# Optimization experiments

Hardware: AMD Instinct MI355X
Metric: run time of the kernel (lower is better)

The kernel has to match this reference:

```python
import jax, jax.numpy as jnp
import numpy as np

DIM = 2048
N_HEADS = 16
N_KV_HEADS = 4
HEAD_DIM = DIM // N_HEADS  # 128
B, S = 2, 2048


def setup_inputs() -> dict:
    key = jax.random.key(0)
    ks = jax.random.split(key, 7)
    x = jax.random.normal(ks[0], (B, S, DIM), dtype=jnp.float32)
    # rotary tables: freqs_cis = exp(i * t * theta), theta_j = 1/10000^(2j/head_dim)
    inv_freq = 1.0 / (10000.0 ** (np.arange(0, HEAD_DIM, 2, dtype=np.float32) / HEAD_DIM))
    t = np.arange(S, dtype=np.float32)
    angles = jnp.asarray(np.outer(t, inv_freq))  # [S, HEAD_DIM//2]
    freqs_cos = jnp.cos(angles)
    freqs_sin = jnp.sin(angles)
    # Linear weights stored [in, out] (torch Linear applies x @ W.T; equivalent math)
    sd = 1.0 / np.sqrt(DIM)
    wq = jax.random.uniform(ks[1], (DIM, N_HEADS * HEAD_DIM), jnp.float32, -sd, sd)
    wk = jax.random.uniform(ks[2], (DIM, N_KV_HEADS * HEAD_DIM), jnp.float32, -sd, sd)
    wv = jax.random.uniform(ks[3], (DIM, N_KV_HEADS * HEAD_DIM), jnp.float32, -sd, sd)
    wo = jax.random.uniform(ks[4], (N_HEADS * HEAD_DIM, DIM), jnp.float32, -sd, sd)
    return {"x": x, "freqs_cos": freqs_cos, "freqs_sin": freqs_sin,
            "wq": wq, "wk": wk, "wv": wv, "wo": wo}


def _apply_rotary(xq, xk, cos, sin):
    # xq: [B,S,H,D], xk: [B,S,KH,D]; cos/sin: [S, D//2]
    def rot(t):
        tr = t.reshape(*t.shape[:-1], -1, 2)  # [..., D//2, 2] (real, imag)
        r, i = tr[..., 0], tr[..., 1]
        c = cos[None, :, None, :]
        s = sin[None, :, None, :]
        out_r = r * c - i * s
        out_i = r * s + i * c
        return jnp.stack([out_r, out_i], axis=-1).reshape(t.shape)
    return rot(xq), rot(xk)


def reference(x, freqs_cos, freqs_sin, wq, wk, wv, wo):
    bsz, seqlen, _ = x.shape
    xq = (x @ wq).reshape(bsz, seqlen, N_HEADS, HEAD_DIM)
    xk = (x @ wk).reshape(bsz, seqlen, N_KV_HEADS, HEAD_DIM)
    xv = (x @ wv).reshape(bsz, seqlen, N_KV_HEADS, HEAD_DIM)
    xq, xk = _apply_rotary(xq, xk, freqs_cos, freqs_sin)
    rep = N_HEADS // N_KV_HEADS
    xk = jnp.repeat(xk, rep, axis=2)
    xv = jnp.repeat(xv, rep, axis=2)
    # [B,H,S,D]
    q = xq.transpose(0, 2, 1, 3)
    k = xk.transpose(0, 2, 1, 3)
    v = xv.transpose(0, 2, 1, 3)
    scale = 1.0 / jnp.sqrt(jnp.asarray(HEAD_DIM, dtype=q.dtype))
    scores = jnp.einsum('bhqd,bhkd->bhqk', q, k) * scale
    causal = jnp.tril(jnp.ones((seqlen, seqlen), dtype=bool))
    scores = jnp.where(causal[None, None], scores, jnp.asarray(-jnp.inf, scores.dtype))
    attn = jax.nn.softmax(scores, axis=-1)
    out = jnp.einsum('bhqk,bhkd->bhqd', attn, v)  # [B,H,S,D]
    out = out.transpose(0, 2, 1, 3).reshape(bsz, seqlen, N_HEADS * HEAD_DIM)
    return out @ wo
```

## Files before the change

### kernel.cpp

```cpp
#include <hip/hip_runtime.h>
#include <hip/hip_bf16.h>

typedef unsigned short u16;
typedef unsigned int u32;
typedef __bf16 bf16x8 __attribute__((ext_vector_type(8)));
typedef float f32x4 __attribute__((ext_vector_type(4)));
typedef u32 u32x2 __attribute__((ext_vector_type(2)));

#define AS1 __attribute__((address_space(1)))
#define AS3 __attribute__((address_space(3)))

__device__ __forceinline__ void gload16(const void* gp, void* lp) {
    __builtin_amdgcn_global_load_lds((const AS1 u32*)gp, (AS3 u32*)lp, 16, 0, 0);
}

__device__ __forceinline__ u16 f2b(float f) {
    __bf16 h = (__bf16)f;
    return __builtin_bit_cast(u16, h);
}

__global__ __launch_bounds__(256) void prep_kernel(const float* __restrict__ x,
                                                   const float* __restrict__ wq,
                                                   const float* __restrict__ wk,
                                                   const float* __restrict__ wv,
                                                   const float* __restrict__ wo,
                                                   u16* __restrict__ xb,
                                                   u16* __restrict__ wT,
                                                   u16* __restrict__ woT) {
    __shared__ u16 tile[32][33];
    const int bid = blockIdx.x, tid = threadIdx.x;
    if (bid < 8192) {
        int i = bid * 256 + tid;
        f32x4 v = *(const f32x4*)(x + (size_t)i * 4);
        u32x2 o;
        o[0] = (u32)f2b(v[0]) | ((u32)f2b(v[1]) << 16);
        o[1] = (u32)f2b(v[2]) | ((u32)f2b(v[3]) << 16);
        *(u32x2*)(xb + (size_t)i * 4) = o;
        return;
    }
    const float* in;
    u16* out;
    int C, t;
    if (bid < 12288) { t = bid - 8192; in = wq; out = wT; C = 2048; }
    else if (bid < 13312) { t = bid - 12288; in = wk; out = wT + 2048 * 2048; C = 512; }
    else if (bid < 14336) { t = bid - 13312; in = wv; out = wT + 2560 * 2048; C = 512; }
    else { t = bid - 14336; in = wo; out = woT; C = 2048; }
    const int nbx = C >> 5;
    const int bx = (t % nbx) * 32, by = (t / nbx) * 32;
    const int tx = tid & 31, ty = tid >> 5;
#pragma unroll
    for (int i = 0; i < 32; i += 8)
        tile[ty + i][tx] = f2b(in[(size_t)(by + ty + i) * C + bx + tx]);
    __syncthreads();
#pragma unroll
    for (int i = 0; i < 32; i += 8)
        out[(size_t)(bx + ty + i) * 2048 + by + tx] = tile[tx][ty + i];
}

__global__ __launch_bounds__(256) void transpose_v(const u16* __restrict__ qkv,
                                                   u16* __restrict__ vT) {
    __shared__ u16 tile[32][33];
    const int bx = blockIdx.x * 32;
    const int by = blockIdx.y * 32;
    const int tx = threadIdx.x & 31, ty = threadIdx.x >> 5;
#pragma unroll
    for (int i = 0; i < 32; i += 8)
        tile[ty + i][tx] = qkv[(size_t)(by + ty + i) * 3072 + 2560 + bx + tx];
    __syncthreads();
    const int b = by >> 11, s0 = by & 2047;
#pragma unroll
    for (int i = 0; i < 32; i += 8)
        vT[(size_t)(b * 512 + bx + ty + i) * 2048 + s0 + tx] = tile[tx][ty + i];
}

template <typename OT, bool ROPE>
__global__ __launch_bounds__(256) void gemm_bt(const __bf16* __restrict__ A,
                                               const __bf16* __restrict__ Bt,
                                               OT* __restrict__ C,
                                               int K, int ldc,
                                               const float* __restrict__ fc,
                                               const float* __restrict__ fs) {
    __shared__ __align__(16) __bf16 Al[128 * 32];
    __shared__ __align__(16) __bf16 Bl[128 * 32];
    const int tid = threadIdx.x;
    const int lane = tid & 63, w = tid >> 6;
    const int wm = w >> 1, wn = w & 1;
    const int ln15 = lane & 15, lg = lane >> 4;
    const int nwg = gridDim.x * gridDim.y;
    const int lid = blockIdx.y * gridDim.x + blockIdx.x;
    const int swz = (lid & 7) * (nwg >> 3) + (lid >> 3);
    const int bm = swz / gridDim.x, bn = swz % gridDim.x;

    const f32x4 fzero = {0.f, 0.f, 0.f, 0.f};
    f32x4 acc[4][4];
#pragma unroll
    for (int m = 0; m < 4; m++)
#pragma unroll
        for (int n = 0; n < 4; n++) acc[m][n] = fzero;

    const __bf16* Ab = A + (size_t)(bm * 128) * K;
    const __bf16* Bb = Bt + (size_t)(bn * 128) * K;

    for (int k0 = 0; k0 < K; k0 += 32) {
#pragma unroll
        for (int i = 0; i < 2; i++) {
            int gid = i * 256 + tid;
            int row = gid >> 2, gc = gid & 3;
            gload16(Ab + (size_t)row * K + k0 + gc * 8, (char*)Al + gid * 16);
            gload16(Bb + (size_t)row * K + k0 + gc * 8, (char*)Bl + gid * 16);
        }
        __syncthreads();
        bf16x8 af[4], bfr[4];
#pragma unroll
        for (int m = 0; m < 4; m++)
            af[m] = *(const bf16x8*)&Al[(wm * 64 + m * 16 + ln15) * 32 + lg * 8];
#pragma unroll
        for (int n = 0; n < 4; n++)
            bfr[n] = *(const bf16x8*)&Bl[(wn * 64 + n * 16 + ln15) * 32 + lg * 8];
#pragma unroll
        for (int m = 0; m < 4; m++)
#pragma unroll
            for (int n = 0; n < 4; n++)
                acc[m][n] = __builtin_amdgcn_mfma_f32_16x16x32_bf16(af[m], bfr[n], acc[m][n], 0, 0, 0);
        __syncthreads();
    }

    if (ROPE) {
#pragma unroll
        for (int n = 0; n < 4; n++) {
            const int col = bn * 128 + wn * 64 + n * 16 + ln15;
            if (col < 2560) {
                const int p = (col & 127) >> 1;
                const bool odd = (col & 1) != 0;
#pragma unroll
                for (int m = 0; m < 4; m++)
#pragma unroll
                    for (int r = 0; r < 4; r++) {
                        const int row = bm * 128 + wm * 64 + m * 16 + lg * 4 + r;
                        const int sp = row & 2047;
                        float c = fc[sp * 64 + p];
                        float sn = fs[sp * 64 + p];
                        float v = acc[m][n][r];
                        float v2 = __shfl_xor(v, 1);
                        acc[m][n][r] = odd ? (v2 * sn + v * c) : (v * c - v2 * sn);
                    }
            }
        }
    }

#pragma unroll
    for (int m = 0; m < 4; m++)
#pragma unroll
        for (int n = 0; n < 4; n++)
#pragma unroll
            for (int r = 0; r < 4; r++) {
                int row = bm * 128 + wm * 64 + m * 16 + lg * 4 + r;
                int col = bn * 128 + wn * 64 + n * 16 + ln15;
                C[(size_t)row * ldc + col] = (OT)acc[m][n][r];
            }
}

__global__ __launch_bounds__(512) void attn_kernel(const __bf16* __restrict__ qkv,
                                                   const __bf16* __restrict__ vT,
                                                   __bf16* __restrict__ ctx) {
    __shared__ __align__(16) __bf16 Klds[2][64 * 128];
    __shared__ __align__(16) __bf16 VTlds[2][128 * 64];
    __shared__ __align__(16) __bf16 Plds[8][16 * 64];

    const int tid = threadIdx.x, lane = tid & 63, w = tid >> 6;
    const int ln15 = lane & 15, lg = lane >> 4;
    int i = blockIdx.x, qblk, hb;
    if (i < 256) { qblk = 15 - (i >> 5); hb = i & 31; }
    else { int j = i - 256; qblk = j >> 5; hb = j & 31; }
    const int h = hb >> 1, b = hb & 1;
    const int kvh = h >> 2;
    const int qw0 = qblk * 128 + w * 16;
    const float c1 = 0.08838834764831845f * 1.4426950408889634f;

    const __bf16* qbase = qkv + (size_t)(b * 2048 + qw0 + ln15) * 3072 + h * 128;
    bf16x8 aq[4];
#pragma unroll
    for (int c = 0; c < 4; c++)
        aq[c] = *(const bf16x8*)(qbase + c * 32 + lg * 8);

    const __bf16* Kg = qkv + (size_t)(b * 2048) * 3072 + 2048 + kvh * 128;
    const __bf16* Vg = vT + (size_t)((b * 4 + kvh) * 128) * 2048;

    const f32x4 fzero = {0.f, 0.f, 0.f, 0.f};
    float m_run[4], l_run[4];
    f32x4 acc[8];
#pragma unroll
    for (int r = 0; r < 4; r++) { m_run[r] = -1e30f; l_run[r] = 0.f; }
#pragma unroll
    for (int dt = 0; dt < 8; dt++) acc[dt] = fzero;

    const int nt = 2 * qblk + 2;

#define STAGE(buf, t)                                                                     \
    do {                                                                                  \
        const int kb_ = (t) * 64;                                                         \
        _Pragma("unroll") for (int i2 = 0; i2 < 2; i2++) {                                \
            int gid = i2 * 512 + tid;                                                     \
            int kv = gid >> 4, sl = gid & 15;                                             \
            gload16(Kg + (size_t)(kb_ + kv) * 3072 + ((sl ^ (kv & 7)) * 8),               \
                    (char*)Klds[buf] + gid * 16);                                         \
        }                                                                                 \
        _Pragma("unroll") for (int i2 = 0; i2 < 2; i2++) {                                \
            int gid = i2 * 512 + tid;                                                     \
            int d = gid >> 3, sl = gid & 7;                                               \
            gload16(Vg + (size_t)d * 2048 + kb_ + ((sl ^ (d & 7)) * 8),                   \
                    (char*)VTlds[buf] + gid * 16);                                        \
        }                                                                                 \
    } while (0)

    STAGE(0, 0);
    __syncthreads();

    for (int t = 0; t < nt; t++) {
        const int cur = t & 1;
        const int kbase = t * 64;
        if (t + 1 < nt) STAGE(cur ^ 1, t + 1);

        if (kbase <= qw0 + 15) {
            f32x4 st[4];
#pragma unroll
            for (int ct = 0; ct < 4; ct++) {
                int kv = ct * 16 + ln15;
                f32x4 s = fzero;
#pragma unroll
                for (int c = 0; c < 4; c++) {
                    int g = c * 4 + lg;
                    bf16x8 bk = *(const bf16x8*)&Klds[cur][kv * 128 + ((g ^ (kv & 7)) * 8)];
                    s = __builtin_amdgcn_mfma_f32_16x16x32_bf16(aq[c], bk, s, 0, 0, 0);
                }
                st[ct] = s;
            }
            if (kbase + 63 > qw0) {
#pragma unroll
                for (int ct = 0; ct < 4; ct++) {
                    int kvi = kbase + ct * 16 + ln15;
#pragma unroll
                    for (int r = 0; r < 4; r++) {
                        int qi = qw0 + lg * 4 + r;
                        if (kvi > qi) st[ct][r] = -1e30f;
                    }
                }
            }
            float tm[4];
#pragma unroll
            for (int r = 0; r < 4; r++)
                tm[r] = fmaxf(fmaxf(st[0][r], st[1][r]), fmaxf(st[2][r], st[3][r]));
#pragma unroll
            for (int off = 1; off < 16; off <<= 1)
#pragma unroll
                for (int r = 0; r < 4; r++)
                    tm[r] = fmaxf(tm[r], __shfl_xor(tm[r], off, 16));
            float corr[4];
#pragma unroll
            for (int r = 0; r < 4; r++) {
                float mn = fmaxf(m_run[r], tm[r]);
                corr[r] = exp2f((m_run[r] - mn) * c1);
                m_run[r] = mn;
            }
            float ts[4];
#pragma unroll
            for (int r = 0; r < 4; r++) {
                const int q = lg * 4 + r;
                float s = 0.f;
#pragma unroll
                for (int ct = 0; ct < 4; ct++) {
                    float p = exp2f((st[ct][r] - m_run[r]) * c1);
                    s += p;
                    int pg = ct * 2 + (ln15 >> 3);
                    Plds[w][q * 64 + ((pg ^ (q & 7)) * 8) + (ln15 & 7)] = (__bf16)p;
                }
                ts[r] = s;
            }
#pragma unroll
            for (int off = 1; off < 16; off <<= 1)
#pragma unroll
                for (int r = 0; r < 4; r++)
                    ts[r] += __shfl_xor(ts[r], off, 16);
#pragma unroll
            for (int r = 0; r < 4; r++) l_run[r] = l_run[r] * corr[r] + ts[r];
#pragma unroll
            for (int dt = 0; dt < 8; dt++)
#pragma unroll
                for (int r = 0; r < 4; r++) acc[dt][r] *= corr[r];
#pragma unroll
            for (int s2 = 0; s2 < 2; s2++) {
                const int kvg = s2 * 4 + lg;
                bf16x8 pa = *(const bf16x8*)&Plds[w][ln15 * 64 + ((kvg ^ (ln15 & 7)) * 8)];
#pragma unroll
                for (int dt = 0; dt < 8; dt++) {
                    int d = dt * 16 + ln15;
                    bf16x8 bv = *(const bf16x8*)&VTlds[cur][d * 64 + ((kvg ^ (d & 7)) * 8)];
                    acc[dt] = __builtin_amdgcn_mfma_f32_16x16x32_bf16(pa, bv, acc[dt], 0, 0, 0);
                }
            }
        }
        __syncthreads();
    }
#undef STAGE

    __bf16* crow = ctx + (size_t)(b * 2048 + qw0) * 2048 + h * 128;
#pragma unroll
    for (int dt = 0; dt < 8; dt++)
#pragma unroll
        for (int r = 0; r < 4; r++) {
            float v = acc[dt][r] / l_run[r];
            crow[(size_t)(lg * 4 + r) * 2048 + dt * 16 + ln15] = (__bf16)v;
        }
}

extern "C" void kernel_launch(void* const* d_in, const int* in_sizes, int n_in,
                              void* d_out, int out_size, void* d_ws, size_t ws_size,
                              hipStream_t stream) {
    const float* x = (const float*)d_in[0];
    const float* fc = (const float*)d_in[1];
    const float* fs = (const float*)d_in[2];
    const float* wq = (const float*)d_in[3];
    const float* wk = (const float*)d_in[4];
    const float* wv = (const float*)d_in[5];
    const float* wo = (const float*)d_in[6];
    float* out = (float*)d_out;

    char* ws = (char*)d_ws;
    __bf16* wT  = (__bf16*)ws;
    __bf16* woT = (__bf16*)(ws + 12582912);
    __bf16* xb  = (__bf16*)(ws + 20971520);
    __bf16* qkv = (__bf16*)(ws + 37748736);
    __bf16* ctx = (__bf16*)(ws + 62914560);
    __bf16* vT  = xb;

    prep_kernel<<<18432, 256, 0, stream>>>(x, wq, wk, wv, wo, (u16*)xb, (u16*)wT, (u16*)woT);

    gemm_bt<__bf16, true><<<dim3(24, 32), 256, 0, stream>>>(xb, wT, qkv, 2048, 3072, fc, fs);

    transpose_v<<<dim3(16, 128), 256, 0, stream>>>((const u16*)qkv, (u16*)vT);

    attn_kernel<<<512, 512, 0, stream>>>(qkv, vT, ctx);

    gemm_bt<float, false><<<dim3(16, 32), 256, 0, stream>>>(ctx, woT, out, 2048, 2048, nullptr, nullptr);
}
```

Measured before the change: 399.5 us.

## Compute transposed S tiles and pass P through register shuffles, not LDS

The QK^T MFMA operands are swapped so each lane holds one query row's scores across kv positions. Row max and row sum then need only two cross-lane shuffles instead of 16-lane butterfly reductions per row. The probability tile is packed to bf16 with v_cvt_pk_bf16_f32 and rearranged into the PV A-operand layout with ds_bpermute shuffles, removing the per-wave Plds scratch and its store/load round trip. In exchange it adds many shuffles and selects per iteration, and correction factors must be broadcast back to the accumulator row layout.

```diff
diff --git a/kernel.cpp b/kernel.cpp
--- a/kernel.cpp
+++ b/kernel.cpp
@@ -6,6 +6,7 @@
 typedef __bf16 bf16x8 __attribute__((ext_vector_type(8)));
 typedef float f32x4 __attribute__((ext_vector_type(4)));
 typedef u32 u32x2 __attribute__((ext_vector_type(2)));
+typedef u32 u32x4 __attribute__((ext_vector_type(4)));
 
 #define AS1 __attribute__((address_space(1)))
 #define AS3 __attribute__((address_space(3)))
@@ -17,6 +18,12 @@
 __device__ __forceinline__ u16 f2b(float f) {
     __bf16 h = (__bf16)f;
     return __builtin_bit_cast(u16, h);
+}
+
+__device__ __forceinline__ u32 cvtpk(float lo, float hi) {
+    u32 d;
+    asm("v_cvt_pk_bf16_f32 %0, %1, %2" : "=v"(d) : "v"(lo), "v"(hi));
+    return d;
 }
 
 __global__ __launch_bounds__(256) void prep_kernel(const float* __restrict__ x,
@@ -165,10 +172,9 @@
                                                    __bf16* __restrict__ ctx) {
     __shared__ __align__(16) __bf16 Klds[2][64 * 128];
     __shared__ __align__(16) __bf16 VTlds[2][128 * 64];
-    __shared__ __align__(16) __bf16 Plds[8][16 * 64];
 
     const int tid = threadIdx.x, lane = tid & 63, w = tid >> 6;
-    const int ln15 = lane & 15, lg = lane >> 4;
+    const int ln15 = lane & 15, lg = (lane >> 4) & 3;
     int i = blockIdx.x, qblk, hb;
     if (i < 256) { qblk = 15 - (i >> 5); hb = i & 31; }
     else { int j = i - 256; qblk = j >> 5; hb = j & 31; }
@@ -187,12 +193,14 @@
     const __bf16* Vg = vT + (size_t)((b * 4 + kvh) * 128) * 2048;
 
     const f32x4 fzero = {0.f, 0.f, 0.f, 0.f};
-    float m_run[4], l_run[4];
+    float m_run = -1e30f, l_run = 0.f;
     f32x4 acc[8];
 #pragma unroll
-    for (int r = 0; r < 4; r++) { m_run[r] = -1e30f; l_run[r] = 0.f; }
-#pragma unroll
     for (int dt = 0; dt < 8; dt++) acc[dt] = fzero;
+
+    const int L0 = ln15 + ((lane & 16) << 1);
+    const int L1 = L0 + 16;
+    const bool selhi = (lane & 32) != 0;
 
     const int nt = 2 * qblk + 2;
 
@@ -231,66 +239,74 @@
                 for (int c = 0; c < 4; c++) {
                     int g = c * 4 + lg;
                     bf16x8 bk = *(const bf16x8*)&Klds[cur][kv * 128 + ((g ^ (kv & 7)) * 8)];
-                    s = __builtin_amdgcn_mfma_f32_16x16x32_bf16(aq[c], bk, s, 0, 0, 0);
+                    s = __builtin_amdgcn_mfma_f32_16x16x32_bf16(bk, aq[c], s, 0, 0, 0);
                 }
                 st[ct] = s;
             }
             if (kbase + 63 > qw0) {
-#pragma unroll
-                for (int ct = 0; ct < 4; ct++) {
-                    int kvi = kbase + ct * 16 + ln15;
+                const int qi = qw0 + ln15;
+#pragma unroll
+                for (int ct = 0; ct < 4; ct++)
 #pragma unroll
                     for (int r = 0; r < 4; r++) {
-                        int qi = qw0 + lg * 4 + r;
+                        int kvi = kbase + ct * 16 + lg * 4 + r;
                         if (kvi > qi) st[ct][r] = -1e30f;
                     }
+            }
+            f32x4 t4 = st[0];
+#pragma unroll
+            for (int ct = 1; ct < 4; ct++)
+#pragma unroll
+                for (int r = 0; r < 4; r++) t4[r] = fmaxf(t4[r], st[ct][r]);
+            float m0 = fmaxf(fmaxf(t4[0], t4[1]), fmaxf(t4[2], t4[3]));
+            m0 = fmaxf(m0, __shfl_xor(m0, 16));
+            m0 = fmaxf(m0, __shfl_xor(m0, 32));
+            float mn = fmaxf(m_run, m0);
+            float corr = exp2f((m_run - mn) * c1);
+            m_run = mn;
+            float p[4][4];
+            f32x4 s4 = fzero;
+#pragma unroll
+            for (int ct = 0; ct < 4; ct++)
+#pragma unroll
+                for (int r = 0; r < 4; r++) {
+                    p[ct][r] = exp2f((st[ct][r] - mn) * c1);
+                    s4[r] += p[ct][r];
                 }
-            }
-            float tm[4];
-#pragma unroll
-            for (int r = 0; r < 4; r++)
-                tm[r] = fmaxf(fmaxf(st[0][r], st[1][r]), fmaxf(st[2][r], st[3][r]));
-#pragma unroll
-            for (int off = 1; off < 16; off <<= 1)
-#pragma unroll
-                for (int r = 0; r < 4; r++)
-                    tm[r] = fmaxf(tm[r], __shfl_xor(tm[r], off, 16));
-            float corr[4];
-#pragma unroll
-            for (int r = 0; r < 4; r++) {
-                float mn = fmaxf(m_run[r], tm[r]);
-                corr[r] = exp2f((m_run[r] - mn) * c1);
-                m_run[r] = mn;
-            }
-            float ts[4];
-#pragma unroll
-            for (int r = 0; r < 4; r++) {
-                const int q = lg * 4 + r;
-                float s = 0.f;
-#pragma unroll
-                for (int ct = 0; ct < 4; ct++) {
-                    float p = exp2f((st[ct][r] - m_run[r]) * c1);
-                    s += p;
-                    int pg = ct * 2 + (ln15 >> 3);
-                    Plds[w][q * 64 + ((pg ^ (q & 7)) * 8) + (ln15 & 7)] = (__bf16)p;
-                }
-                ts[r] = s;
-            }
-#pragma unroll
-            for (int off = 1; off < 16; off <<= 1)
-#pragma unroll
-                for (int r = 0; r < 4; r++)
-                    ts[r] += __shfl_xor(ts[r], off, 16);
-#pragma unroll
-            for (int r = 0; r < 4; r++) l_run[r] = l_run[r] * corr[r] + ts[r];
+            float ssum = (s4[0] + s4[1]) + (s4[2] + s4[3]);
+            ssum += __shfl_xor(ssum, 16);
+            ssum += __shfl_xor(ssum, 32);
+            l_run = l_run * corr + ssum;
+            u32 P32[4][2];
+#pragma unroll
+            for (int ct = 0; ct < 4; ct++) {
+                P32[ct][0] = cvtpk(p[ct][0], p[ct][1]);
+                P32[ct][1] = cvtpk(p[ct][2], p[ct][3]);
+            }
+            float corrR[4];
+#pragma unroll
+            for (int r = 0; r < 4; r++) corrR[r] = __shfl(corr, lg * 4 + r);
 #pragma unroll
             for (int dt = 0; dt < 8; dt++)
 #pragma unroll
-                for (int r = 0; r < 4; r++) acc[dt][r] *= corr[r];
+                for (int r = 0; r < 4; r++) acc[dt][r] *= corrR[r];
 #pragma unroll
             for (int s2 = 0; s2 < 2; s2++) {
+                int b00 = __shfl((int)P32[s2 * 2][0], L0);
+                int b01 = __shfl((int)P32[s2 * 2][1], L0);
+                int b10 = __shfl((int)P32[s2 * 2 + 1][0], L0);
+                int b11 = __shfl((int)P32[s2 * 2 + 1][1], L0);
+                int c00 = __shfl((int)P32[s2 * 2][0], L1);
+                int c01 = __shfl((int)P32[s2 * 2][1], L1);
+                int c10 = __shfl((int)P32[s2 * 2 + 1][0], L1);
+                int c11 = __shfl((int)P32[s2 * 2 + 1][1], L1);
+                u32x4 av;
+                av[0] = selhi ? (u32)b10 : (u32)b00;
+                av[1] = selhi ? (u32)b11 : (u32)b01;
+                av[2] = selhi ? (u32)c10 : (u32)c00;
+                av[3] = selhi ? (u32)c11 : (u32)c01;
+                bf16x8 pa = __builtin_bit_cast(bf16x8, av);
                 const int kvg = s2 * 4 + lg;
-                bf16x8 pa = *(const bf16x8*)&Plds[w][ln15 * 64 + ((kvg ^ (ln15 & 7)) * 8)];
 #pragma unroll
                 for (int dt = 0; dt < 8; dt++) {
                     int d = dt * 16 + ln15;
@@ -303,12 +319,15 @@
     }
 #undef STAGE
 
+    float lR[4];
+#pragma unroll
+    for (int r = 0; r < 4; r++) lR[r] = __shfl(l_run, lg * 4 + r);
     __bf16* crow = ctx + (size_t)(b * 2048 + qw0) * 2048 + h * 128;
 #pragma unroll
     for (int dt = 0; dt < 8; dt++)
 #pragma unroll
         for (int r = 0; r < 4; r++) {
-            float v = acc[dt][r] / l_run[r];
+            float v = acc[dt][r] / lR[r];
             crow[(size_t)(lg * 4 + r) * 2048 + dt * 16 + ln15] = (__bf16)v;
         }
 }
```

Result: faster. 373.6 us (-6.5%).
